# Kernel optimization log

Hardware: AMD Instinct MI355X
Metric: run time of the kernel (lower is better)

## Reference

```python
import jax, jax.numpy as jnp
import numpy as np

MINI_BLOCK = 4

def setup_inputs() -> dict:
    key = jax.random.key(0)
    k1, k2 = jax.random.split(key)
    B, IN, OUT = 4096, 4096, 4096
    gy, gx = OUT // MINI_BLOCK, IN // MINI_BLOCK
    x = jax.random.normal(k1, (B, IN), dtype=jnp.float32)
    eigens = jax.random.normal(k2, (gy, gx, MINI_BLOCK), dtype=jnp.float32)
    return {"x": x, "eigens": eigens}

def reference(x, eigens):
    # Block-circulant linear: out[b, y, :] = sum_x circconv(eigens[y, x], x_blk[b, x])
    # computed in the frequency domain. Original code used two-sided rfft +
    # complex_mult + irfft per (b, y, x) block and summed over x; since the FFT
    # and complex product are linear, we contract over x in frequency space
    # with an einsum instead of materializing the (B, gy, gx, block) tensor.
    gy, gx, blk = eigens.shape
    xb = x.reshape(-1, gx, blk)                      # (B, gx, blk)
    f_eig = jnp.fft.rfft(eigens, axis=-1)            # (gy, gx, blk//2+1) complex
    f_x = jnp.fft.rfft(xb, axis=-1)                  # (B, gx, blk//2+1)
    f_out = jnp.einsum('yxk,bxk->byk', f_eig, f_x)   # contract over gx
    out = jnp.fft.irfft(f_out, n=blk, axis=-1)       # (B, gy, blk)
    return out.reshape(-1, gy * blk)
```

## Files before the change

kernel.cpp:

```cpp
#include <hip/hip_runtime.h>


typedef __attribute__((ext_vector_type(8))) short bf16x8_t;
typedef __attribute__((ext_vector_type(4))) float f32x4_t;

#define NDIM 4096
#define TILE 128
#define BK 32

__device__ __forceinline__ unsigned short f2bf(float f) {
    unsigned int u = __builtin_bit_cast(unsigned int, f);
    u += 0x7fffu + ((u >> 16) & 1u);
    return (unsigned short)(u >> 16);
}

__device__ __forceinline__ void async_copy16(const void* g, void* l) {
    __builtin_amdgcn_global_load_lds(
        (const __attribute__((address_space(1))) void*)g,
        (__attribute__((address_space(3))) void*)l,
        16, 0, 0);
}


__global__ __launch_bounds__(256) void pre_k(const float* __restrict__ x,
                                             const float* __restrict__ eig,
                                             unsigned short* __restrict__ xp,
                                             unsigned short* __restrict__ B) {
    const int t = threadIdx.x;
    if (blockIdx.x < 4096) {
        int gid = blockIdx.x * 256 + t;
        int b = gid >> 8, j0 = (gid & 255) << 2;
        const float4* src = (const float4*)x + ((size_t)b << 10) + j0;
        unsigned short S[4], R[4], Mi[4], Z[4], T[4];
#pragma unroll
        for (int q = 0; q < 4; ++q) {
            float4 v = src[q];
            float r = v.x - v.z, m = v.w - v.y;
            S[q]  = f2bf(r + m);
            R[q]  = f2bf(r);
            Mi[q] = f2bf(m);
            Z[q]  = f2bf(v.x + v.y + v.z + v.w);
            T[q]  = f2bf(v.x - v.y + v.z - v.w);
        }
        unsigned short* dst = xp + (size_t)b * 5120 + j0;
        *(ushort4*)(dst)        = *(const ushort4*)S;
        *(ushort4*)(dst + 1024) = *(const ushort4*)R;
        *(ushort4*)(dst + 2048) = *(const ushort4*)Mi;
        *(ushort4*)(dst + 3072) = *(const ushort4*)Z;
        *(ushort4*)(dst + 4096) = *(const ushort4*)T;
    } else {
        int gid = (blockIdx.x - 4096) * 256 + t;
        int y = gid >> 8, c0 = (gid & 255) << 2;
        const float4* src = (const float4*)eig + ((size_t)y << 10) + c0;
        unsigned short P0[4], P1[4], P2[4], P3[4], P4[4];
#pragma unroll
        for (int q = 0; q < 4; ++q) {
            float4 v = src[q];
            float r = v.x - v.z, m = v.w - v.y;
            P0[q] = f2bf(r);
            P1[q] = f2bf(m - r);
            P2[q] = f2bf(-(m + r));
            P3[q] = f2bf(v.x + v.y + v.z + v.w);
            P4[q] = f2bf(v.x - v.y + v.z - v.w);
        }
        unsigned short* dst = B + (size_t)y * 5120 + c0;
        *(ushort4*)(dst)        = *(const ushort4*)P0;
        *(ushort4*)(dst + 1024) = *(const ushort4*)P1;
        *(ushort4*)(dst + 2048) = *(const ushort4*)P2;
        *(ushort4*)(dst + 3072) = *(const ushort4*)P3;
        *(ushort4*)(dst + 4096) = *(const ushort4*)P4;
    }
}

__global__ __launch_bounds__(512, 2) void gemm_f(
        const unsigned short* __restrict__ A,
        const unsigned short* __restrict__ B,
        float* __restrict__ C) {
    __shared__ unsigned short sm[2][16384];

    const int raw    = blockIdx.x;
    const int xcd    = raw & 7;
    const int idx    = raw >> 3;
    const int rowBlk = xcd * 4 + (idx >> 3);
    const int colBlk = idx & 7;

    const int t    = threadIdx.x;
    const int lane = t & 63;
    const int w    = t >> 6;
    const int wm   = (w >> 2) * 64;
    const int wn   = (w & 3) * 32;
    const int lr   = lane & 15;
    const int quad = lane >> 4;
    const int xr   = lr & 7;

    const int srow = t >> 3;
    const int scol = ((t & 7) ^ ((t >> 3) & 7)) << 3;
    const unsigned short* pa0 = A + (size_t)(rowBlk * 128 + srow) * 5120 + scol;
    const unsigned short* pa1 = pa0 + (size_t)64 * 5120;
    const unsigned short* pb0 = B + (size_t)(colBlk * 128 + srow) * 5120 + scol;
    const unsigned short* pb1 = pb0 + (size_t)64 * 5120;

    char* smb  = (char*)&sm[0][0];
    char* dstT = smb + (size_t)t * 16;

    int koff = 0;
    int cur  = 0;

    f32x4_t aK1[4][2] = {};
    f32x4_t aOi[4][2];
    f32x4_t aO0[4][2] = {};
    f32x4_t aO2[4][2] = {};

#define STAGE_F(BUF)                                           \
    {                                                          \
        char* d = dstT + (BUF) * 32768;                        \
        async_copy16(pa0 + koff, d);                           \
        async_copy16(pa1 + koff, d + 8192);                    \
        async_copy16(pb0 + koff, d + 16384);                   \
        async_copy16(pb1 + koff, d + 24576);                   \
        koff += 64;                                            \
    }

#define COMPUTE_F(BUF, ACC)                                                   \
    {                                                                         \
        const char* ab = smb + (BUF) * 32768 + (wm + lr) * 128;               \
        const char* bb = smb + (BUF) * 32768 + 16384 + (wn + lr) * 128;       \
        _Pragma("unroll")                                                     \
        for (int kk = 0; kk < 2; ++kk) {                                      \
            const int sw = ((((kk << 2) | quad)) ^ xr) << 4;                  \
            bf16x8_t af[4], bfv[2];                                           \
            _Pragma("unroll")                                                 \
            for (int i = 0; i < 4; ++i)                                       \
                af[i] = *(const bf16x8_t*)(ab + i * 2048 + sw);               \
            _Pragma("unroll")                                                 \
            for (int j = 0; j < 2; ++j)                                       \
                bfv[j] = *(const bf16x8_t*)(bb + j * 2048 + sw);              \
            _Pragma("unroll")                                                 \
            for (int mt = 0; mt < 4; ++mt)                                    \
                _Pragma("unroll")                                             \
                for (int nt = 0; nt < 2; ++nt)                                \
                    ACC[mt][nt] = __builtin_amdgcn_mfma_f32_16x16x32_bf16(    \
                        af[mt], bfv[nt], ACC[mt][nt], 0, 0, 0);               \
        }                                                                     \
    }

#define PHASE_F(ACC, ISLAST)                                   \
    _Pragma("unroll 2")                                        \
    for (int s2 = 0; s2 < 16; ++s2) {                          \
        if (!(ISLAST) || s2 < 15) STAGE_F(cur ^ 1);            \
        COMPUTE_F(cur, ACC);                                   \
        asm volatile("s_waitcnt vmcnt(0)" ::: "memory");       \
        __syncthreads();                                       \
        cur ^= 1;                                              \
    }

    STAGE_F(0);
    asm volatile("s_waitcnt vmcnt(0)" ::: "memory");
    __syncthreads();

    PHASE_F(aK1, 0)
#pragma unroll
    for (int mt = 0; mt < 4; ++mt)
#pragma unroll
        for (int nt = 0; nt < 2; ++nt) aOi[mt][nt] = aK1[mt][nt];
    PHASE_F(aOi, 0)
    PHASE_F(aK1, 0)
    PHASE_F(aO0, 0)
    PHASE_F(aO2, 1)

#undef PHASE_F
#undef COMPUTE_F
#undef STAGE_F

    const int orow0 = rowBlk * 128 + wm + quad * 4;
    const int yc0   = colBlk * 128 + wn + lr;
#pragma unroll
    for (int mt = 0; mt < 4; ++mt) {
#pragma unroll
        for (int r = 0; r < 4; ++r) {
            float* dst = C + (size_t)(orow0 + mt * 16 + r) * NDIM;
#pragma unroll
            for (int nt = 0; nt < 2; ++nt) {
                int yc = yc0 + nt * 16;
                float O0 = aO0[mt][nt][r], Or = aK1[mt][nt][r];
                float Oi = aOi[mt][nt][r], O2 = aO2[mt][nt][r];
                float4 o;
                o.x = 0.25f * (O0 + 2.0f * Or + O2);
                o.y = 0.25f * (O0 - 2.0f * Oi - O2);
                o.z = 0.25f * (O0 - 2.0f * Or + O2);
                o.w = 0.25f * (O0 + 2.0f * Oi - O2);
                *(float4*)(dst + 4 * yc) = o;
            }
        }
    }
}


__global__ __launch_bounds__(256) void fwd_x_fb(const float* __restrict__ x,
                                                unsigned short* __restrict__ xp) {
    int gid = blockIdx.x * 256 + threadIdx.x;
    int b = gid >> 10, j = gid & 1023;
    float4 v = ((const float4*)x)[(size_t)b * 1024 + j];
    unsigned short* dst = xp + (size_t)b * NDIM + j;
    dst[0]    = f2bf(v.x + v.y + v.z + v.w);
    dst[1024] = f2bf(v.x - v.z);
    dst[2048] = f2bf(v.w - v.y);
    dst[3072] = f2bf(v.x - v.y + v.z - v.w);
}

__global__ __launch_bounds__(256) void build_b_fb(const float* __restrict__ eig,
                                                  unsigned short* __restrict__ B) {
    int gid = blockIdx.x * 256 + threadIdx.x;
    int y = gid >> 10, c = gid & 1023;
    float4 v = ((const float4*)eig)[(size_t)y * 1024 + c];
    float r = v.x - v.z, s = v.w - v.y;
    B[(size_t)y * 1024 + c] = f2bf(v.x + v.y + v.z + v.w);
    unsigned short* b1r = B + 1048576 + (size_t)y * 2048;
    b1r[c]        = f2bf(r);
    b1r[1024 + c] = f2bf(-s);
    unsigned short* b1i = B + 3145728 + (size_t)y * 2048;
    b1i[c]        = f2bf(s);
    b1i[1024 + c] = f2bf(r);
    B[5242880 + (size_t)y * 1024 + c] = f2bf(v.x - v.y + v.z - v.w);
}

__global__ __launch_bounds__(256, 2) void gemm_fb(
        const unsigned short* __restrict__ A,
        const unsigned short* __restrict__ B,
        float* __restrict__ C) {
    __shared__ unsigned short lA[TILE * BK];
    __shared__ unsigned short lB[TILE * BK];

    const int Ks[4]   = {1024, 2048, 2048, 1024};
    const int Aoff[4] = {0, 1024, 1024, 3072};
    const size_t Boff[4] = {0u, 1048576u, 3145728u, 5242880u};

    int lin = blockIdx.x;
    int seg, nseg, blkM;
    if (lin < 512) { seg = 1 + ((lin >> 3) & 1); nseg = lin & 7; blkM = lin >> 4; }
    else { int i = lin - 512; seg = ((i >> 3) & 1) * 3; nseg = i & 7; blkM = i >> 4; }

    const int K    = Ks[seg];
    const int aoff = Aoff[seg];
    const unsigned short* Bs = B + Boff[seg];

    const int t    = threadIdx.x;
    const int lane = t & 63;
    const int w    = t >> 6;
    const int wm   = (w >> 1) * 64;
    const int wn   = (w & 1) * 64;
    const int lr   = lane & 15;
    const int quad = lane >> 4;

    const int e0 = t * 8;
    const int r0 = e0 >> 5;
    const int c0 = e0 & 31;

    const unsigned short* pa0 = A + (size_t)(blkM * TILE + r0) * NDIM + aoff + c0;
    const unsigned short* pa1 = pa0 + (size_t)64 * NDIM;
    const unsigned short* pb0 = Bs + (size_t)(nseg * TILE + r0) * K + c0;
    const unsigned short* pb1 = pb0 + (size_t)64 * K;

    unsigned short* dA0 = &lA[e0];
    unsigned short* dA1 = &lA[2048 + e0];
    unsigned short* dB0 = &lB[e0];
    unsigned short* dB1 = &lB[2048 + e0];

    const unsigned short* la0 = &lA[(wm + lr) * BK + quad * 8];
    const unsigned short* lb0 = &lB[(wn + lr) * BK + quad * 8];

    f32x4_t acc[4][4] = {};

    for (int k0 = 0; k0 < K; k0 += BK) {
        async_copy16(pa0 + k0, dA0);
        async_copy16(pa1 + k0, dA1);
        async_copy16(pb0 + k0, dB0);
        async_copy16(pb1 + k0, dB1);
        asm volatile("s_waitcnt vmcnt(0)" ::: "memory");
        __syncthreads();

        bf16x8_t af[4], bfr[4];
#pragma unroll
        for (int i = 0; i < 4; ++i)
            af[i] = *(const bf16x8_t*)(la0 + i * 16 * BK);
#pragma unroll
        for (int i = 0; i < 4; ++i)
            bfr[i] = *(const bf16x8_t*)(lb0 + i * 16 * BK);

#pragma unroll
        for (int mt = 0; mt < 4; ++mt)
#pragma unroll
            for (int nt = 0; nt < 4; ++nt)
                acc[mt][nt] = __builtin_amdgcn_mfma_f32_16x16x32_bf16(
                    af[mt], bfr[nt], acc[mt][nt], 0, 0, 0);

        __syncthreads();
    }

    const int orow0 = blkM * TILE + wm + quad * 4;
    const int ocol0 = seg * 1024 + nseg * TILE + wn + lr;
#pragma unroll
    for (int mt = 0; mt < 4; ++mt) {
#pragma unroll
        for (int r = 0; r < 4; ++r) {
            float* dst = C + (size_t)(orow0 + mt * 16 + r) * NDIM + ocol0;
#pragma unroll
            for (int nt = 0; nt < 4; ++nt)
                dst[nt * 16] = acc[mt][nt][r];
        }
    }
}

__global__ __launch_bounds__(256) void post_fb(float* __restrict__ O) {
    float* row = O + (size_t)blockIdx.x * NDIM;
    const int t = threadIdx.x;
    float4 v0 = *(const float4*)(row + 4 * t);
    float4 vr = *(const float4*)(row + 1024 + 4 * t);
    float4 vi = *(const float4*)(row + 2048 + 4 * t);
    float4 v2 = *(const float4*)(row + 3072 + 4 * t);
    __syncthreads();
    const float* a0 = (const float*)&v0;
    const float* ar = (const float*)&vr;
    const float* ai = (const float*)&vi;
    const float* a2 = (const float*)&v2;
#pragma unroll
    for (int i = 0; i < 4; ++i) {
        float4 o;
        o.x = 0.25f * (a0[i] + 2.0f * ar[i] + a2[i]);
        o.y = 0.25f * (a0[i] - 2.0f * ai[i] - a2[i]);
        o.z = 0.25f * (a0[i] - 2.0f * ar[i] + a2[i]);
        o.w = 0.25f * (a0[i] + 2.0f * ai[i] - a2[i]);
        *(float4*)(row + 16 * t + 4 * i) = o;
    }
}


extern "C" void kernel_launch(void* const* d_in, const int* in_sizes, int n_in,
                              void* d_out, int out_size, void* d_ws, size_t ws_size,
                              hipStream_t stream) {
    const float* x   = (const float*)d_in[0];
    const float* eig = (const float*)d_in[1];
    float* out = (float*)d_out;

    const size_t NEED = (size_t)50 * 1024 * 1024;

    if (ws_size >= NEED) {
        unsigned short* Xp = (unsigned short*)d_ws;
        unsigned short* Bp = (unsigned short*)((char*)d_ws + 41943040u);

        pre_k<<<5120, 256, 0, stream>>>(x, eig, Xp, Bp);
        gemm_f<<<256, 512, 0, stream>>>(Xp, Bp, out);
    } else {
        unsigned short* Xp = (unsigned short*)d_ws;
        unsigned short* Bp = Xp + (size_t)NDIM * NDIM;

        fwd_x_fb<<<(NDIM * 1024) / 256, 256, 0, stream>>>(x, Xp);
        build_b_fb<<<(1024 * 1024) / 256, 256, 0, stream>>>(eig, Bp);
        gemm_fb<<<dim3(1024, 1), 256, 0, stream>>>(Xp, Bp, out);
        post_fb<<<NDIM, 256, 0, stream>>>(out);
    }
}
```

Before: 188.3 us.

## Triple-buffer LDS pipeline with partial vmcnt waits and MFMA priority boost

```diff
diff --git a/kernel.cpp b/kernel.cpp
--- a/kernel.cpp
+++ b/kernel.cpp
@@ -76,7 +76,7 @@
         const unsigned short* __restrict__ A,
         const unsigned short* __restrict__ B,
         float* __restrict__ C) {
-    __shared__ unsigned short sm[2][16384];
+    __shared__ unsigned short sm[3][16384];
 
     const int raw    = blockIdx.x;
     const int xcd    = raw & 7;
@@ -104,16 +104,15 @@
     char* dstT = smb + (size_t)t * 16;
 
     int koff = 0;
-    int cur  = 0;
 
     f32x4_t aK1[4][2] = {};
     f32x4_t aOi[4][2];
     f32x4_t aO0[4][2] = {};
     f32x4_t aO2[4][2] = {};
 
-#define STAGE_F(BUF)                                           \
+#define STAGE_F(BOFF)                                          \
     {                                                          \
-        char* d = dstT + (BUF) * 32768;                        \
+        char* d = dstT + (BOFF);                               \
         async_copy16(pa0 + koff, d);                           \
         async_copy16(pa1 + koff, d + 8192);                    \
         async_copy16(pb0 + koff, d + 16384);                   \
@@ -121,10 +120,10 @@
         koff += 64;                                            \
     }
 
-#define COMPUTE_F(BUF, ACC)                                                   \
+#define COMPUTE_F(BOFF, ACC)                                                  \
     {                                                                         \
-        const char* ab = smb + (BUF) * 32768 + (wm + lr) * 128;               \
-        const char* bb = smb + (BUF) * 32768 + 16384 + (wn + lr) * 128;       \
+        const char* ab = smb + (BOFF) + (wm + lr) * 128;                      \
+        const char* bb = smb + (BOFF) + 16384 + (wn + lr) * 128;              \
         _Pragma("unroll")                                                     \
         for (int kk = 0; kk < 2; ++kk) {                                      \
             const int sw = ((((kk << 2) | quad)) ^ xr) << 4;                  \
@@ -135,40 +134,55 @@
             _Pragma("unroll")                                                 \
             for (int j = 0; j < 2; ++j)                                       \
                 bfv[j] = *(const bf16x8_t*)(bb + j * 2048 + sw);              \
+            __builtin_amdgcn_s_setprio(1);                                    \
             _Pragma("unroll")                                                 \
             for (int mt = 0; mt < 4; ++mt)                                    \
                 _Pragma("unroll")                                             \
                 for (int nt = 0; nt < 2; ++nt)                                \
                     ACC[mt][nt] = __builtin_amdgcn_mfma_f32_16x16x32_bf16(    \
                         af[mt], bfv[nt], ACC[mt][nt], 0, 0, 0);               \
+            __builtin_amdgcn_s_setprio(0);                                    \
         }                                                                     \
     }
 
-#define PHASE_F(ACC, ISLAST)                                   \
-    _Pragma("unroll 2")                                        \
-    for (int s2 = 0; s2 < 16; ++s2) {                          \
-        if (!(ISLAST) || s2 < 15) STAGE_F(cur ^ 1);            \
-        COMPUTE_F(cur, ACC);                                   \
-        asm volatile("s_waitcnt vmcnt(0)" ::: "memory");       \
-        __syncthreads();                                       \
-        cur ^= 1;                                              \
-    }
+#define STEP_F(ACC)                                            \
+    {                                                          \
+        asm volatile("s_waitcnt vmcnt(4)" ::: "memory");       \
+        __builtin_amdgcn_s_barrier();                          \
+        __builtin_amdgcn_sched_barrier(0);                     \
+        int sb_ = cb + 65536;                                  \
+        if (sb_ >= 98304) sb_ -= 98304;                        \
+        if (koff < 5120) STAGE_F(sb_);                         \
+        COMPUTE_F(cb, ACC);                                    \
+        cb += 32768;                                           \
+        if (cb >= 98304) cb = 0;                               \
+    }
+
+#define PHASE_F(ACC, NSTEP)                                    \
+    _Pragma("unroll 1")                                        \
+    for (int s2 = 0; s2 < (NSTEP); ++s2) STEP_F(ACC)
 
     STAGE_F(0);
+    STAGE_F(32768);
+    int cb = 0;
+
+    PHASE_F(aK1, 16)
+#pragma unroll
+    for (int mt = 0; mt < 4; ++mt)
+#pragma unroll
+        for (int nt = 0; nt < 2; ++nt) aOi[mt][nt] = aK1[mt][nt];
+    PHASE_F(aOi, 16)
+    PHASE_F(aK1, 16)
+    PHASE_F(aO0, 16)
+    PHASE_F(aO2, 15)
+
     asm volatile("s_waitcnt vmcnt(0)" ::: "memory");
-    __syncthreads();
-
-    PHASE_F(aK1, 0)
-#pragma unroll
-    for (int mt = 0; mt < 4; ++mt)
-#pragma unroll
-        for (int nt = 0; nt < 2; ++nt) aOi[mt][nt] = aK1[mt][nt];
-    PHASE_F(aOi, 0)
-    PHASE_F(aK1, 0)
-    PHASE_F(aO0, 0)
-    PHASE_F(aO2, 1)
+    __builtin_amdgcn_s_barrier();
+    __builtin_amdgcn_sched_barrier(0);
+    COMPUTE_F(cb, aO2);
 
 #undef PHASE_F
+#undef STEP_F
 #undef COMPUTE_F
 #undef STAGE_F
 
```

New measurement: 184.0 us. 1.02x faster.
